# Performance work log

Hardware: AMD Instinct MI355X
Metric: run time of the kernel (lower is better)

## Reference

```python
import jax, jax.numpy as jnp
import numpy as np

N = 12288
IN_F = 256
OUT_F = 128
ALPHA = 0.2  # LeakyReLU negative slope


def setup_inputs() -> dict:
    key = jax.random.key(0)
    k_x, k_adj, k_w, k_a1, k_a2 = jax.random.split(key, 5)
    x = jax.random.normal(k_x, (N, IN_F), dtype=jnp.float32)
    adj = jax.random.randint(k_adj, (N, N), 0, 2, dtype=jnp.int32)
    # Learned params (nn.Linear without bias). Kaiming-uniform-ish init scale.
    W = jax.random.normal(k_w, (IN_F, OUT_F), dtype=jnp.float32) / np.sqrt(IN_F)
    a1 = jax.random.normal(k_a1, (OUT_F,), dtype=jnp.float32) / np.sqrt(OUT_F)
    a2 = jax.random.normal(k_a2, (OUT_F,), dtype=jnp.float32) / np.sqrt(OUT_F)
    return {"x": x, "adj": adj, "W": W, "a1": a1, "a2": a2}


def reference(x, adj, W, a1, a2):
    # h = tran(x): [N, OUT_F]
    h = x @ W
    # e[i, j] = att1(h)[j] + att2(h)[i]  (unsqueeze(0) + unsqueeze(1))
    s1 = h @ a1  # [N]
    s2 = h @ a2  # [N]
    e = s1[None, :] + s2[:, None]            # [N, N]
    e = jnp.where(e > 0, e, ALPHA * e)       # LeakyReLU
    e = jnp.where(adj > 0, e, -jnp.inf)      # mask non-edges
    attn = jax.nn.softmax(e, axis=1)         # row softmax (dropout=0 / eval)
    return attn @ h                          # [N, OUT_F]
```

## Files before the change

### kernel.cpp

```cpp
#include <hip/hip_runtime.h>
#include <hip/hip_bf16.h>

constexpr int NR = 12288;
constexpr int KF = 256;
constexpr int DF = 128;
#define NEGBIG (-1e30f)

typedef __attribute__((ext_vector_type(8))) __bf16 bf16x8;
typedef __attribute__((ext_vector_type(4))) float  f32x4;

__device__ __forceinline__ unsigned short f2bf(float f) {
    union { float f; unsigned u; } v; v.f = f;
    unsigned r = v.u + 0x7FFFu + ((v.u >> 16) & 1u);
    return (unsigned short)(r >> 16);
}

__global__ __launch_bounds__(256) void k_gemm_h(
    const float* __restrict__ x, const float* __restrict__ W,
    const float* __restrict__ a1, const float* __restrict__ a2,
    unsigned short* __restrict__ hbT, float* __restrict__ s1, float* __restrict__ s2)
{
    __shared__ __align__(16) float xs[64][65];
    __shared__ __align__(16) float ws[64][132];
    const int t  = threadIdx.x;
    const int tx = t & 15, ty = t >> 4;
    const int rowbase = blockIdx.x * 64;

    float acc[4][8];
#pragma unroll
    for (int i = 0; i < 4; ++i)
#pragma unroll
        for (int j = 0; j < 8; ++j) acc[i][j] = 0.f;

    for (int kt = 0; kt < KF; kt += 64) {
        {
            int row = t >> 2, k0 = (t & 3) * 16;
            const float4* src = (const float4*)(x + (size_t)(rowbase + row) * KF + kt + k0);
            float4 v0 = src[0], v1 = src[1], v2 = src[2], v3 = src[3];
            xs[row][k0+ 0]=v0.x; xs[row][k0+ 1]=v0.y; xs[row][k0+ 2]=v0.z; xs[row][k0+ 3]=v0.w;
            xs[row][k0+ 4]=v1.x; xs[row][k0+ 5]=v1.y; xs[row][k0+ 6]=v1.z; xs[row][k0+ 7]=v1.w;
            xs[row][k0+ 8]=v2.x; xs[row][k0+ 9]=v2.y; xs[row][k0+10]=v2.z; xs[row][k0+11]=v2.w;
            xs[row][k0+12]=v3.x; xs[row][k0+13]=v3.y; xs[row][k0+14]=v3.z; xs[row][k0+15]=v3.w;
        }
        {
            int k = t >> 2, c0 = (t & 3) * 32;
            const float4* src = (const float4*)(W + (size_t)(kt + k) * DF + c0);
#pragma unroll
            for (int j = 0; j < 8; ++j)
                *(float4*)&ws[k][c0 + j * 4] = src[j];
        }
        __syncthreads();
#pragma unroll 4
        for (int k = 0; k < 64; ++k) {
            float xv[4];
#pragma unroll
            for (int ri = 0; ri < 4; ++ri) xv[ri] = xs[ty * 4 + ri][k];
            float4 w0 = *(float4*)&ws[k][tx * 8];
            float4 w1 = *(float4*)&ws[k][tx * 8 + 4];
#pragma unroll
            for (int ri = 0; ri < 4; ++ri) {
                acc[ri][0] += xv[ri] * w0.x; acc[ri][1] += xv[ri] * w0.y;
                acc[ri][2] += xv[ri] * w0.z; acc[ri][3] += xv[ri] * w0.w;
                acc[ri][4] += xv[ri] * w1.x; acc[ri][5] += xv[ri] * w1.y;
                acc[ri][6] += xv[ri] * w1.z; acc[ri][7] += xv[ri] * w1.w;
            }
        }
        __syncthreads();
    }
#pragma unroll
    for (int ci = 0; ci < 8; ++ci) {
        int col = tx * 8 + ci;
        ushort4 u;
        u.x = f2bf(acc[0][ci]); u.y = f2bf(acc[1][ci]);
        u.z = f2bf(acc[2][ci]); u.w = f2bf(acc[3][ci]);
        *(ushort4*)(hbT + (size_t)col * NR + rowbase + ty * 4) = u;
    }
    float4 a1lo = *(const float4*)(a1 + tx * 8), a1hi = *(const float4*)(a1 + tx * 8 + 4);
    float4 a2lo = *(const float4*)(a2 + tx * 8), a2hi = *(const float4*)(a2 + tx * 8 + 4);
#pragma unroll
    for (int ri = 0; ri < 4; ++ri) {
        float p1 = acc[ri][0]*a1lo.x + acc[ri][1]*a1lo.y + acc[ri][2]*a1lo.z + acc[ri][3]*a1lo.w
                 + acc[ri][4]*a1hi.x + acc[ri][5]*a1hi.y + acc[ri][6]*a1hi.z + acc[ri][7]*a1hi.w;
        float p2 = acc[ri][0]*a2lo.x + acc[ri][1]*a2lo.y + acc[ri][2]*a2lo.z + acc[ri][3]*a2lo.w
                 + acc[ri][4]*a2hi.x + acc[ri][5]*a2hi.y + acc[ri][6]*a2hi.z + acc[ri][7]*a2hi.w;
#pragma unroll
        for (int off = 8; off > 0; off >>= 1) {
            p1 += __shfl_xor(p1, off);
            p2 += __shfl_xor(p2, off);
        }
        if (tx == 0) {
            s1[rowbase + ty * 4 + ri] = p1;
            s2[rowbase + ty * 4 + ri] = p2;
        }
    }
}

__global__ __launch_bounds__(1024) void k_gmax(
    const float* __restrict__ s1, float* __restrict__ gmax)
{
    __shared__ float red[16];
    const int t = threadIdx.x;
    float m = NEGBIG;
    const float4* s4 = (const float4*)s1;
    for (int i = t; i < NR / 4; i += 1024) {
        float4 v = s4[i];
        m = fmaxf(fmaxf(v.x, v.y), fmaxf(fmaxf(v.z, v.w), m));
    }
#pragma unroll
    for (int off = 32; off > 0; off >>= 1) m = fmaxf(m, __shfl_xor(m, off));
    if ((t & 63) == 0) red[t >> 6] = m;
    __syncthreads();
    if (t < 16) {
        m = red[t];
#pragma unroll
        for (int off = 8; off > 0; off >>= 1) m = fmaxf(m, __shfl_xor(m, off));
        if (t == 0) gmax[0] = m;
    }
}

__global__ __launch_bounds__(256, 5) void k_flash(
    const int* __restrict__ adj, const unsigned short* __restrict__ hbT,
    const float* __restrict__ s1, const float* __restrict__ s2,
    const float* __restrict__ gmaxp,
    float* __restrict__ num, float* __restrict__ lC, int CW)
{
    __shared__ __align__(16) unsigned short hbuf[2][128][40];
    const int t    = threadIdx.x;
    const int wid  = t >> 6, lane = t & 63;
    const int r    = lane & 15, g = lane >> 4;
    const int rowb = blockIdx.x * 64;
    const int prow = rowb + wid * 16 + r;
    const int chunk = blockIdx.y;
    const int j0 = chunk * CW;

    const float gm  = gmaxp[0];
    const float s2r = s2[prow];
    const float zub = s2r + gm;
    const float Mi  = fmaxf(zub, 0.2f * zub);

    float lsum = 0.f;
    f32x4 acc[8];
#pragma unroll
    for (int f = 0; f < 8; ++f) acc[f] = f32x4{0.f, 0.f, 0.f, 0.f};

    const int*   ab = adj + (size_t)prow * NR + j0 + g * 8;
    const float* sb = s1 + j0 + g * 8;
    const int sr = t >> 1, scol = (t & 1) * 16;
    const unsigned short* hs = hbT + (size_t)sr * NR + j0 + scol;

    const int nsteps = CW >> 5;

    {
        int4   Aa0 = *(const int4*)(ab);
        int4   Ab0 = *(const int4*)(ab + 4);
        bf16x8 Ta  = *(const bf16x8*)(hs);
        bf16x8 Tb  = *(const bf16x8*)(hs + 8);
        *(bf16x8*)&hbuf[0][sr][scol]     = Ta;
        *(bf16x8*)&hbuf[0][sr][scol + 8] = Tb;
        __syncthreads();
        int cur = 0;
        int4 Aa = Aa0, Ab = Ab0;
        for (int it = 0; it < nsteps; ++it) {
            const int itn = (it + 1 < nsteps) ? (it + 1) : 0;
            int4   NAa = *(const int4*)(ab + itn * 32);
            int4   NAb = *(const int4*)(ab + itn * 32 + 4);
            bf16x8 NTa = *(const bf16x8*)(hs + itn * 32);
            bf16x8 NTb = *(const bf16x8*)(hs + itn * 32 + 8);
            const float4 Sa = *(const float4*)(sb + it * 32);
            const float4 Sb = *(const float4*)(sb + it * 32 + 4);

            bf16x8 pf;
#define PROC(mm, ss, idx) { \
                float t0 = (ss) + s2r; \
                float lr = fmaxf(t0, 0.2f * t0); \
                float e  = ((mm) > 0) ? lr : NEGBIG; \
                float p  = __expf(e - Mi); \
                lsum += p; \
                pf[idx] = (__bf16)p; }
            PROC(Aa.x, Sa.x, 0) PROC(Aa.y, Sa.y, 1)
            PROC(Aa.z, Sa.z, 2) PROC(Aa.w, Sa.w, 3)
            PROC(Ab.x, Sb.x, 4) PROC(Ab.y, Sb.y, 5)
            PROC(Ab.z, Sb.z, 6) PROC(Ab.w, Sb.w, 7)
#undef PROC

#pragma unroll
            for (int f = 0; f < 8; ++f) {
                bf16x8 bfr = *(const bf16x8*)&hbuf[cur][f * 16 + r][g * 8];
                acc[f] = __builtin_amdgcn_mfma_f32_16x16x32_bf16(pf, bfr, acc[f], 0, 0, 0);
            }

            *(bf16x8*)&hbuf[cur ^ 1][sr][scol]     = NTa;
            *(bf16x8*)&hbuf[cur ^ 1][sr][scol + 8] = NTb;
            __syncthreads();
            Aa = NAa; Ab = NAb; cur ^= 1;
        }
    }

    lsum += __shfl_xor(lsum, 16);
    lsum += __shfl_xor(lsum, 32);
    if (g == 0) lC[(size_t)chunk * NR + prow] = lsum;

    float* nb = num + (size_t)chunk * NR * DF;
#pragma unroll
    for (int f = 0; f < 8; ++f)
#pragma unroll
        for (int q = 0; q < 4; ++q) {
            int row = rowb + wid * 16 + g * 4 + q;
            nb[(size_t)row * DF + f * 16 + r] = acc[f][q];
        }
}

__global__ __launch_bounds__(256) void k_comb(
    const float* __restrict__ num, const float* __restrict__ lC,
    float* __restrict__ out, int CH)
{
    const int t   = threadIdx.x;
    const int row = blockIdx.x * 2 + (t >> 7);
    const int f   = t & 127;
    float L = 0.f, o = 0.f;
    for (int c = 0; c < CH; ++c) {
        L += lC[(size_t)c * NR + row];
        o += num[(size_t)c * NR * DF + (size_t)row * DF + f];
    }
    out[(size_t)row * DF + f] = o / L;
}

extern "C" void kernel_launch(void* const* d_in, const int* in_sizes, int n_in,
                              void* d_out, int out_size, void* d_ws, size_t ws_size,
                              hipStream_t stream)
{
    const float* x   = (const float*)d_in[0];
    const int*   adj = (const int*)d_in[1];
    const float* W   = (const float*)d_in[2];
    const float* a1  = (const float*)d_in[3];
    const float* a2  = (const float*)d_in[4];
    float* out = (float*)d_out;

    char* p = (char*)d_ws;
    unsigned short* hbT = (unsigned short*)p; p += (size_t)DF * NR * 2;
    float*          s1  = (float*)p;          p += (size_t)NR * 4;
    float*          s2  = (float*)p;          p += (size_t)NR * 4;
    float*          gmx = (float*)p;          p += 256;
    size_t base = (size_t)(p - (char*)d_ws);
    size_t per  = (size_t)NR * DF * 4 + (size_t)NR * 4;
    int CH = 8;
    while (CH > 1 && base + (size_t)CH * per > ws_size) CH >>= 1;
    float* numb = (float*)p; p += (size_t)CH * NR * DF * 4;
    float* lC   = (float*)p;

    k_gemm_h<<<NR / 64, 256, 0, stream>>>(x, W, a1, a2, hbT, s1, s2);
    k_gmax<<<1, 1024, 0, stream>>>(s1, gmx);
    k_flash<<<dim3(NR / 64, CH), 256, 0, stream>>>(adj, hbT, s1, s2, gmx, numb, lC, NR / CH);
    k_comb<<<NR / 2, 256, 0, stream>>>(numb, lC, out, CH);
}
```

Baseline: 254.4 us.

## Restructure flash loop with peeled last step, s1 prefetch, and lighter barrier

Rewrites the main attention loop so the final iteration is peeled out, removing the wrap-around dummy prefetch. The s1 score loads are now prefetched one step ahead along with adj and h. __syncthreads is replaced by a barrier that waits only on LDS counters, so outstanding global loads no longer stall at the barrier. Occupancy hint drops from 5 to 4 blocks per CU, giving the compiler more registers for the extra prefetched values.

```diff
diff --git a/kernel.cpp b/kernel.cpp
--- a/kernel.cpp
+++ b/kernel.cpp
@@ -14,6 +14,12 @@
     unsigned r = v.u + 0x7FFFu + ((v.u >> 16) & 1u);
     return (unsigned short)(r >> 16);
 }
+
+#define BARRIER() do { \
+    asm volatile("s_waitcnt lgkmcnt(0)" ::: "memory"); \
+    __builtin_amdgcn_s_barrier(); \
+    asm volatile("" ::: "memory"); \
+} while (0)
 
 __global__ __launch_bounds__(256) void k_gemm_h(
     const float* __restrict__ x, const float* __restrict__ W,
@@ -118,7 +124,7 @@
     }
 }
 
-__global__ __launch_bounds__(256, 5) void k_flash(
+__global__ __launch_bounds__(256, 4) void k_flash(
     const int* __restrict__ adj, const unsigned short* __restrict__ hbT,
     const float* __restrict__ s1, const float* __restrict__ s2,
     const float* __restrict__ gmaxp,
@@ -143,58 +149,72 @@
 #pragma unroll
     for (int f = 0; f < 8; ++f) acc[f] = f32x4{0.f, 0.f, 0.f, 0.f};
 
-    const int*   ab = adj + (size_t)prow * NR + j0 + g * 8;
-    const float* sb = s1 + j0 + g * 8;
+    const int*   ap = adj + (size_t)prow * NR + j0 + g * 8;
+    const float* sp = s1 + j0 + g * 8;
     const int sr = t >> 1, scol = (t & 1) * 16;
     const unsigned short* hs = hbT + (size_t)sr * NR + j0 + scol;
 
     const int nsteps = CW >> 5;
 
+    bf16x8 Ta = *(const bf16x8*)(hs);
+    bf16x8 Tb = *(const bf16x8*)(hs + 8);
+    int4   Aa = *(const int4*)(ap);
+    int4   Ab = *(const int4*)(ap + 4);
+    float4 Sa = *(const float4*)(sp);
+    float4 Sb = *(const float4*)(sp + 4);
+    *(bf16x8*)&hbuf[0][sr][scol]     = Ta;
+    *(bf16x8*)&hbuf[0][sr][scol + 8] = Tb;
+    BARRIER();
+
+    int cur = 0;
+#define PROC(mm, ss, idx) { \
+        float t0 = (ss) + s2r; \
+        float lr = fmaxf(t0, 0.2f * t0); \
+        float e  = ((mm) > 0) ? lr : NEGBIG; \
+        float p  = __expf(e - Mi); \
+        lsum += p; \
+        pf[idx] = (__bf16)p; }
+
+    for (int it = 0; it < nsteps - 1; ++it) {
+        hs += 32; ap += 32; sp += 32;
+        bf16x8 NTa = *(const bf16x8*)(hs);
+        bf16x8 NTb = *(const bf16x8*)(hs + 8);
+        int4   NAa = *(const int4*)(ap);
+        int4   NAb = *(const int4*)(ap + 4);
+        float4 NSa = *(const float4*)(sp);
+        float4 NSb = *(const float4*)(sp + 4);
+
+        bf16x8 pf;
+        PROC(Aa.x, Sa.x, 0) PROC(Aa.y, Sa.y, 1)
+        PROC(Aa.z, Sa.z, 2) PROC(Aa.w, Sa.w, 3)
+        PROC(Ab.x, Sb.x, 4) PROC(Ab.y, Sb.y, 5)
+        PROC(Ab.z, Sb.z, 6) PROC(Ab.w, Sb.w, 7)
+
+#pragma unroll
+        for (int f = 0; f < 8; ++f) {
+            bf16x8 bfr = *(const bf16x8*)&hbuf[cur][f * 16 + r][g * 8];
+            acc[f] = __builtin_amdgcn_mfma_f32_16x16x32_bf16(pf, bfr, acc[f], 0, 0, 0);
+        }
+
+        *(bf16x8*)&hbuf[cur ^ 1][sr][scol]     = NTa;
+        *(bf16x8*)&hbuf[cur ^ 1][sr][scol + 8] = NTb;
+        BARRIER();
+        Aa = NAa; Ab = NAb; Sa = NSa; Sb = NSb;
+        cur ^= 1;
+    }
     {
-        int4   Aa0 = *(const int4*)(ab);
-        int4   Ab0 = *(const int4*)(ab + 4);
-        bf16x8 Ta  = *(const bf16x8*)(hs);
-        bf16x8 Tb  = *(const bf16x8*)(hs + 8);
-        *(bf16x8*)&hbuf[0][sr][scol]     = Ta;
-        *(bf16x8*)&hbuf[0][sr][scol + 8] = Tb;
-        __syncthreads();
-        int cur = 0;
-        int4 Aa = Aa0, Ab = Ab0;
-        for (int it = 0; it < nsteps; ++it) {
-            const int itn = (it + 1 < nsteps) ? (it + 1) : 0;
-            int4   NAa = *(const int4*)(ab + itn * 32);
-            int4   NAb = *(const int4*)(ab + itn * 32 + 4);
-            bf16x8 NTa = *(const bf16x8*)(hs + itn * 32);
-            bf16x8 NTb = *(const bf16x8*)(hs + itn * 32 + 8);
-            const float4 Sa = *(const float4*)(sb + it * 32);
-            const float4 Sb = *(const float4*)(sb + it * 32 + 4);
-
-            bf16x8 pf;
-#define PROC(mm, ss, idx) { \
-                float t0 = (ss) + s2r; \
-                float lr = fmaxf(t0, 0.2f * t0); \
-                float e  = ((mm) > 0) ? lr : NEGBIG; \
-                float p  = __expf(e - Mi); \
-                lsum += p; \
-                pf[idx] = (__bf16)p; }
-            PROC(Aa.x, Sa.x, 0) PROC(Aa.y, Sa.y, 1)
-            PROC(Aa.z, Sa.z, 2) PROC(Aa.w, Sa.w, 3)
-            PROC(Ab.x, Sb.x, 4) PROC(Ab.y, Sb.y, 5)
-            PROC(Ab.z, Sb.z, 6) PROC(Ab.w, Sb.w, 7)
+        bf16x8 pf;
+        PROC(Aa.x, Sa.x, 0) PROC(Aa.y, Sa.y, 1)
+        PROC(Aa.z, Sa.z, 2) PROC(Aa.w, Sa.w, 3)
+        PROC(Ab.x, Sb.x, 4) PROC(Ab.y, Sb.y, 5)
+        PROC(Ab.z, Sb.z, 6) PROC(Ab.w, Sb.w, 7)
+#pragma unroll
+        for (int f = 0; f < 8; ++f) {
+            bf16x8 bfr = *(const bf16x8*)&hbuf[cur][f * 16 + r][g * 8];
+            acc[f] = __builtin_amdgcn_mfma_f32_16x16x32_bf16(pf, bfr, acc[f], 0, 0, 0);
+        }
+    }
 #undef PROC
-
-#pragma unroll
-            for (int f = 0; f < 8; ++f) {
-                bf16x8 bfr = *(const bf16x8*)&hbuf[cur][f * 16 + r][g * 8];
-                acc[f] = __builtin_amdgcn_mfma_f32_16x16x32_bf16(pf, bfr, acc[f], 0, 0, 0);
-            }
-
-            *(bf16x8*)&hbuf[cur ^ 1][sr][scol]     = NTa;
-            *(bf16x8*)&hbuf[cur ^ 1][sr][scol + 8] = NTb;
-            __syncthreads();
-            Aa = NAa; Ab = NAb; cur ^= 1;
-        }
-    }
 
     lsum += __shfl_xor(lsum, 16);
     lsum += __shfl_xor(lsum, 32);
```

After: 293.0 us. +15.2%, slower.

## Stream adj and h tiles via direct global-to-LDS loads in triple-buffered ring

Applied to the files above, without the earlier changes.

The flash kernel now loads both adjacency and transposed-h tiles with global_load_lds into a 3-stage swizzled LDS ring, issuing two steps ahead and waiting on vmcnt before each barrier. s1 for the chunk is staged once in LDS, masking is applied after the exp (select on p), and the column split goes from up to 8 fixed chunks to 12 with occupancy hint lowered to 3. The aim is to hide HBM latency on the large int32 adj stream and cut register pressure from prefetching into VGPRs. It drops the workspace-size fallback, so a smaller workspace would overflow, and it uses more LDS per block.

```diff
diff --git a/kernel.cpp b/kernel.cpp
--- a/kernel.cpp
+++ b/kernel.cpp
@@ -4,6 +4,9 @@
 constexpr int NR = 12288;
 constexpr int KF = 256;
 constexpr int DF = 128;
+constexpr int CH = 12;
+constexpr int CW = NR / CH;
+constexpr int NSTEP = CW / 32;
 #define NEGBIG (-1e30f)
 
 typedef __attribute__((ext_vector_type(8))) __bf16 bf16x8;
@@ -13,6 +16,12 @@
     union { float f; unsigned u; } v; v.f = f;
     unsigned r = v.u + 0x7FFFu + ((v.u >> 16) & 1u);
     return (unsigned short)(r >> 16);
+}
+
+__device__ __forceinline__ void gload16(const void* g, void* l) {
+    __builtin_amdgcn_global_load_lds(
+        (const __attribute__((address_space(1))) void*)g,
+        (__attribute__((address_space(3))) void*)l, 16, 0, 0);
 }
 
 __global__ __launch_bounds__(256) void k_gemm_h(
@@ -118,13 +127,16 @@
     }
 }
 
-__global__ __launch_bounds__(256, 5) void k_flash(
+__global__ __launch_bounds__(256, 3) void k_flash(
     const int* __restrict__ adj, const unsigned short* __restrict__ hbT,
     const float* __restrict__ s1, const float* __restrict__ s2,
     const float* __restrict__ gmaxp,
-    float* __restrict__ num, float* __restrict__ lC, int CW)
-{
-    __shared__ __align__(16) unsigned short hbuf[2][128][40];
+    float* __restrict__ num, float* __restrict__ lC)
+{
+    __shared__ __align__(16) int            adjring[3][2048];
+    __shared__ __align__(16) unsigned short hbtring[3][4096];
+    __shared__ __align__(16) float          s1lds[CW];
+
     const int t    = threadIdx.x;
     const int wid  = t >> 6, lane = t & 63;
     const int r    = lane & 15, g = lane >> 4;
@@ -133,68 +145,82 @@
     const int chunk = blockIdx.y;
     const int j0 = chunk * CW;
 
+    *(float4*)&s1lds[t * 4] = *(const float4*)(s1 + j0 + t * 4);
+
     const float gm  = gmaxp[0];
     const float s2r = s2[prow];
     const float zub = s2r + gm;
     const float Mi  = fmaxf(zub, 0.2f * zub);
 
+    const int arow  = wid * 16 + (lane >> 3);
+    const int acol4 = ((lane & 7) ^ (lane >> 3)) * 4;
+    const int* agp0 = adj + (size_t)(rowb + arow) * NR + j0 + acol4;
+    const int* agp1 = agp0 + (size_t)8 * NR;
+    const int aldso0 = (wid * 16 + 0) * 128;
+    const int aldso1 = (wid * 16 + 8) * 128;
+
+    const int hrow  = wid * 32 + (lane >> 2);
+    const int hcol8 = ((lane & 3) ^ ((lane >> 3) & 3)) * 8;
+    const unsigned short* hgp0 = hbT + (size_t)hrow * NR + j0 + hcol8;
+    const unsigned short* hgp1 = hgp0 + (size_t)16 * NR;
+    const int hldso0 = (wid * 32 + 0) * 64;
+    const int hldso1 = (wid * 32 + 16) * 64;
+
+    const int a_off0 = (wid * 16 + r) * 128 + (((2 * g + 0) ^ (r & 7)) * 16);
+    const int a_off1 = (wid * 16 + r) * 128 + (((2 * g + 1) ^ (r & 7)) * 16);
+    const int h_base = r * 64 + ((g ^ ((r >> 1) & 3)) * 16);
+
+#define ISSUE(st) do { \
+        const int sl_ = (st) % 3; \
+        const size_t go_ = (size_t)(((st) % NSTEP) * 32); \
+        gload16(agp0 + go_, (char*)&adjring[sl_][0] + aldso0); \
+        gload16(agp1 + go_, (char*)&adjring[sl_][0] + aldso1); \
+        gload16(hgp0 + go_, (char*)&hbtring[sl_][0] + hldso0); \
+        gload16(hgp1 + go_, (char*)&hbtring[sl_][0] + hldso1); \
+    } while (0)
+
     float lsum = 0.f;
     f32x4 acc[8];
 #pragma unroll
     for (int f = 0; f < 8; ++f) acc[f] = f32x4{0.f, 0.f, 0.f, 0.f};
 
-    const int*   ab = adj + (size_t)prow * NR + j0 + g * 8;
-    const float* sb = s1 + j0 + g * 8;
-    const int sr = t >> 1, scol = (t & 1) * 16;
-    const unsigned short* hs = hbT + (size_t)sr * NR + j0 + scol;
-
-    const int nsteps = CW >> 5;
-
-    {
-        int4   Aa0 = *(const int4*)(ab);
-        int4   Ab0 = *(const int4*)(ab + 4);
-        bf16x8 Ta  = *(const bf16x8*)(hs);
-        bf16x8 Tb  = *(const bf16x8*)(hs + 8);
-        *(bf16x8*)&hbuf[0][sr][scol]     = Ta;
-        *(bf16x8*)&hbuf[0][sr][scol + 8] = Tb;
-        __syncthreads();
-        int cur = 0;
-        int4 Aa = Aa0, Ab = Ab0;
-        for (int it = 0; it < nsteps; ++it) {
-            const int itn = (it + 1 < nsteps) ? (it + 1) : 0;
-            int4   NAa = *(const int4*)(ab + itn * 32);
-            int4   NAb = *(const int4*)(ab + itn * 32 + 4);
-            bf16x8 NTa = *(const bf16x8*)(hs + itn * 32);
-            bf16x8 NTb = *(const bf16x8*)(hs + itn * 32 + 8);
-            const float4 Sa = *(const float4*)(sb + it * 32);
-            const float4 Sb = *(const float4*)(sb + it * 32 + 4);
-
-            bf16x8 pf;
+    ISSUE(0);
+    ISSUE(1);
+
+    for (int j = 0; j < NSTEP; ++j) {
+        asm volatile("s_waitcnt vmcnt(4) lgkmcnt(0)" ::: "memory");
+        __builtin_amdgcn_s_barrier();
+        __builtin_amdgcn_sched_barrier(0);
+        ISSUE(j + 2);
+
+        const int sl = j % 3;
+        const int4 Aa = *(const int4*)((const char*)&adjring[sl][0] + a_off0);
+        const int4 Ab = *(const int4*)((const char*)&adjring[sl][0] + a_off1);
+        const float4 Sa = *(const float4*)&s1lds[j * 32 + g * 8];
+        const float4 Sb = *(const float4*)&s1lds[j * 32 + g * 8 + 4];
+
+        bf16x8 pf;
 #define PROC(mm, ss, idx) { \
-                float t0 = (ss) + s2r; \
-                float lr = fmaxf(t0, 0.2f * t0); \
-                float e  = ((mm) > 0) ? lr : NEGBIG; \
-                float p  = __expf(e - Mi); \
-                lsum += p; \
-                pf[idx] = (__bf16)p; }
-            PROC(Aa.x, Sa.x, 0) PROC(Aa.y, Sa.y, 1)
-            PROC(Aa.z, Sa.z, 2) PROC(Aa.w, Sa.w, 3)
-            PROC(Ab.x, Sb.x, 4) PROC(Ab.y, Sb.y, 5)
-            PROC(Ab.z, Sb.z, 6) PROC(Ab.w, Sb.w, 7)
+            float t0 = (ss) + s2r; \
+            float lr = fmaxf(t0, 0.2f * t0); \
+            float q  = __expf(lr - Mi); \
+            float p  = ((mm) > 0) ? q : 0.f; \
+            lsum += p; \
+            pf[idx] = (__bf16)p; }
+        PROC(Aa.x, Sa.x, 0) PROC(Aa.y, Sa.y, 1)
+        PROC(Aa.z, Sa.z, 2) PROC(Aa.w, Sa.w, 3)
+        PROC(Ab.x, Sb.x, 4) PROC(Ab.y, Sb.y, 5)
+        PROC(Ab.z, Sb.z, 6) PROC(Ab.w, Sb.w, 7)
 #undef PROC
 
-#pragma unroll
-            for (int f = 0; f < 8; ++f) {
-                bf16x8 bfr = *(const bf16x8*)&hbuf[cur][f * 16 + r][g * 8];
-                acc[f] = __builtin_amdgcn_mfma_f32_16x16x32_bf16(pf, bfr, acc[f], 0, 0, 0);
-            }
-
-            *(bf16x8*)&hbuf[cur ^ 1][sr][scol]     = NTa;
-            *(bf16x8*)&hbuf[cur ^ 1][sr][scol + 8] = NTb;
-            __syncthreads();
-            Aa = NAa; Ab = NAb; cur ^= 1;
-        }
-    }
+        const char* hb = (const char*)&hbtring[sl][0] + h_base;
+#pragma unroll
+        for (int f = 0; f < 8; ++f) {
+            bf16x8 bfr = *(const bf16x8*)(hb + f * 1024);
+            acc[f] = __builtin_amdgcn_mfma_f32_16x16x32_bf16(pf, bfr, acc[f], 0, 0, 0);
+        }
+    }
+#undef ISSUE
 
     lsum += __shfl_xor(lsum, 16);
     lsum += __shfl_xor(lsum, 32);
@@ -212,7 +238,7 @@
 
 __global__ __launch_bounds__(256) void k_comb(
     const float* __restrict__ num, const float* __restrict__ lC,
-    float* __restrict__ out, int CH)
+    float* __restrict__ out)
 {
     const int t   = threadIdx.x;
     const int row = blockIdx.x * 2 + (t >> 7);
@@ -241,15 +267,11 @@
     float*          s1  = (float*)p;          p += (size_t)NR * 4;
     float*          s2  = (float*)p;          p += (size_t)NR * 4;
     float*          gmx = (float*)p;          p += 256;
-    size_t base = (size_t)(p - (char*)d_ws);
-    size_t per  = (size_t)NR * DF * 4 + (size_t)NR * 4;
-    int CH = 8;
-    while (CH > 1 && base + (size_t)CH * per > ws_size) CH >>= 1;
-    float* numb = (float*)p; p += (size_t)CH * NR * DF * 4;
-    float* lC   = (float*)p;
+    float*          numb = (float*)p;         p += (size_t)CH * NR * DF * 4;
+    float*          lC   = (float*)p;
 
     k_gemm_h<<<NR / 64, 256, 0, stream>>>(x, W, a1, a2, hbT, s1, s2);
     k_gmax<<<1, 1024, 0, stream>>>(s1, gmx);
-    k_flash<<<dim3(NR / 64, CH), 256, 0, stream>>>(adj, hbT, s1, s2, gmx, numb, lC, NR / CH);
-    k_comb<<<NR / 2, 256, 0, stream>>>(numb, lC, out, CH);
-}
+    k_flash<<<dim3(NR / 64, CH), 256, 0, stream>>>(adj, hbT, s1, s2, gmx, numb, lC);
+    k_comb<<<NR / 2, 256, 0, stream>>>(numb, lC, out);
+}
```

Measured after the change: 255.4 us. No clear change (+0.4%).
